# Optimization experiments

Hardware: AMD Instinct MI355X
Metric: run time of the kernel (lower is better)

Reference implementation:

```python
import jax, jax.numpy as jnp
import numpy as np

N_NODES = 100000
N_EDGES = 1600000
F_IN = 500
HIDDEN = 64
N_CLASS = 40


def gcn_conv(x, W, b, src, dst, n_nodes):
    """PyG GCNConv: add self-loops, symmetric deg^-1/2 normalization,
    linear transform then scatter-add aggregation at dst."""
    h = x @ W  # [N, out]
    loop = jnp.arange(n_nodes, dtype=src.dtype)
    s = jnp.concatenate([src, loop])  # sources incl. self-loops
    d = jnp.concatenate([dst, loop])
    deg = jax.ops.segment_sum(jnp.ones_like(d, dtype=h.dtype), d, num_segments=n_nodes)
    dinv = jnp.where(deg > 0, jax.lax.rsqrt(deg), 0.0)
    norm = dinv[s] * dinv[d]  # [E+N]
    msg = h[s] * norm[:, None]  # gather + scale, [E+N, out]
    out = jax.ops.segment_sum(msg, d, num_segments=n_nodes)
    return out + b


def setup_inputs() -> dict:
    key = jax.random.key(0)
    k1, k2, k3, k4 = jax.random.split(key, 4)
    x = jax.random.normal(k1, (N_NODES, F_IN), dtype=jnp.float32)
    edge_index = jax.random.randint(k2, (2, N_EDGES), 0, N_NODES, dtype=jnp.int64)
    # Glorot-style init for GCNConv weights
    W1 = jax.random.normal(k3, (F_IN, HIDDEN), dtype=jnp.float32) / np.sqrt(F_IN)
    b1 = jnp.zeros((HIDDEN,), dtype=jnp.float32)
    W2 = jax.random.normal(k4, (HIDDEN, N_CLASS), dtype=jnp.float32) / np.sqrt(HIDDEN)
    b2 = jnp.zeros((N_CLASS,), dtype=jnp.float32)
    return {"x": x, "W1": W1, "b1": b1, "W2": W2, "b2": b2, "edge_index": edge_index}


def reference(x, W1, b1, W2, b2, edge_index):
    src, dst = edge_index[0], edge_index[1]
    n = x.shape[0]
    h = jax.nn.relu(gcn_conv(x, W1, b1, src, dst, n))
    # dropout is identity in eval mode (F.dropout with training=False)
    out = gcn_conv(h, W2, b2, src, dst, n)
    return jax.nn.log_softmax(out, axis=1)
```

## Files before the change

### kernel.cpp

```cpp
#include <hip/hip_runtime.h>
#include <math.h>

#define N_NODES 100000
#define N_EDGES 1600000
#define F_IN    500
#define HIDDEN  64
#define N_CLASS 40
#define KPAD    512

#define NB   2048
#define NPB  49
#define EPB  16384
#define CAP  1536

typedef __attribute__((ext_vector_type(4))) float f32x4;
typedef __attribute__((ext_vector_type(8))) __bf16 bf16x8;

__device__ __forceinline__ unsigned short f2bf(float f) {
    unsigned int u = __float_as_uint(f);
    u = (u + 0x7FFF + ((u >> 16) & 1)) >> 16;
    return (unsigned short)u;
}
__device__ __forceinline__ unsigned int packbf(float a, float b) {
    return (unsigned int)f2bf(a) | ((unsigned int)f2bf(b) << 16);
}
__device__ __forceinline__ float bfu_lo(unsigned int v) {
    return __uint_as_float(v << 16);
}
__device__ __forceinline__ float bfu_hi(unsigned int v) {
    return __uint_as_float(v & 0xFFFF0000u);
}

__global__ void k_prep_w1t(const float* __restrict__ w1, unsigned short* __restrict__ w1t,
                           int* __restrict__ bcnt) {
    int idx = blockIdx.x * blockDim.x + threadIdx.x;
    if (idx < NB) bcnt[idx] = 0;
    if (idx >= HIDDEN * KPAD) return;
    int n = idx >> 9, k = idx & (KPAD - 1);
    float v = (k < F_IN) ? w1[k * HIDDEN + n] : 0.f;
    w1t[idx] = f2bf(v);
}

__launch_bounds__(1024)
__global__ void k_bhist(const int* __restrict__ dst, int* __restrict__ bcnt, int e) {
    __shared__ int h[NB];
    for (int i = threadIdx.x; i < NB; i += 1024) h[i] = 0;
    __syncthreads();
    int base = blockIdx.x * EPB;
#pragma unroll
    for (int j = 0; j < 16; ++j) {
        int i = base + j * 1024 + threadIdx.x;
        if (i < e) atomicAdd(&h[dst[i] / NPB], 1);
    }
    __syncthreads();
    for (int i = threadIdx.x; i < NB; i += 1024)
        if (h[i]) atomicAdd(&bcnt[i], h[i]);
}

__launch_bounds__(1024)
__global__ void k_bscan(const int* __restrict__ bcnt, int* __restrict__ bptr,
                        int* __restrict__ bcur) {
    __shared__ int s[1024];
    int t = threadIdx.x;
    int a = bcnt[2 * t], b = bcnt[2 * t + 1];
    int v = a + b;
    s[t] = v;
    __syncthreads();
    for (int off = 1; off < 1024; off <<= 1) {
        int u = (t >= off) ? s[t - off] : 0;
        __syncthreads();
        s[t] += u;
        __syncthreads();
    }
    int excl = s[t] - v;
    bptr[2 * t] = excl;     bptr[2 * t + 1] = excl + a;
    bcur[2 * t] = excl;     bcur[2 * t + 1] = excl + a;
    if (t == 1023) bptr[NB] = s[1023];
}

__launch_bounds__(1024)
__global__ void k_bfill(const int* __restrict__ src, const int* __restrict__ dst,
                        int* __restrict__ bcur, int2* __restrict__ ebuf, int e) {
    __shared__ int hist[NB];
    __shared__ int base_[NB];
    for (int i = threadIdx.x; i < NB; i += 1024) hist[i] = 0;
    __syncthreads();
    int b0 = blockIdx.x * EPB;
    int s_[16], d_[16];
#pragma unroll
    for (int j = 0; j < 16; ++j) {
        int i = b0 + j * 1024 + threadIdx.x;
        if (i < e) {
            s_[j] = src[i];
            d_[j] = dst[i];
            atomicAdd(&hist[d_[j] / NPB], 1);
        } else d_[j] = -1;
    }
    __syncthreads();
    for (int i = threadIdx.x; i < NB; i += 1024) {
        int hc = hist[i];
        base_[i] = hc ? atomicAdd(&bcur[i], hc) : 0;
        hist[i] = 0;
    }
    __syncthreads();
#pragma unroll
    for (int j = 0; j < 16; ++j) {
        if (d_[j] >= 0) {
            int bu = d_[j] / NPB;
            int r = atomicAdd(&hist[bu], 1);
            ebuf[base_[bu] + r] = make_int2(s_[j], d_[j]);
        }
    }
}

__launch_bounds__(256)
__global__ void k_bucket_csr(const int2* __restrict__ ebuf, const int* __restrict__ bptr,
                             int* __restrict__ rp, int* __restrict__ col,
                             float* __restrict__ dinv, int n) {
    int b  = blockIdx.x;
    int lo = b * NPB;
    if (lo >= n) return;
    int hi  = min(lo + NPB, n);
    int eb0 = bptr[b], ec = bptr[b + 1] - eb0;

    __shared__ int2 pairs[CAP];
    __shared__ int  hist[NPB];
    __shared__ int  excl[NPB + 1];
    for (int j = threadIdx.x; j < NPB; j += 256) hist[j] = 0;
    __syncthreads();
    for (int i = threadIdx.x; i < ec; i += 256) {
        int2 p = ebuf[eb0 + i];
        if (i < CAP) pairs[i] = p;
        atomicAdd(&hist[p.y - lo], 1);
    }
    __syncthreads();
    if (threadIdx.x == 0) {
        int acc = 0;
        for (int j = 0; j < NPB; ++j) { excl[j] = acc; acc += hist[j]; }
        excl[NPB] = acc;
    }
    __syncthreads();
    for (int j = threadIdx.x; j < hi - lo; j += 256) {
        rp[lo + j]   = eb0 + excl[j];
        dinv[lo + j] = rsqrtf((float)(hist[j] + 1));
    }
    if (hi == n && threadIdx.x == 0) rp[n] = eb0 + ec;
    __syncthreads();
    for (int j = threadIdx.x; j < NPB; j += 256) hist[j] = 0;
    __syncthreads();
    for (int i = threadIdx.x; i < ec; i += 256) {
        int2 p  = (i < CAP) ? pairs[i] : ebuf[eb0 + i];
        int  li = p.y - lo;
        int  r  = atomicAdd(&hist[li], 1);
        col[eb0 + excl[li] + r] = p.x;
    }
}

__launch_bounds__(256)
__global__ void k_gemm1(const float* __restrict__ x, const unsigned short* __restrict__ w1t,
                        const float* __restrict__ dinv, unsigned short* __restrict__ hs, int n) {
    const int tid  = threadIdx.x;
    const int wave = tid >> 6;
    const int lane = tid & 63;
    const int quad = lane >> 4;
    const int l16  = lane & 15;
    const int rowb = blockIdx.x * 64 + wave * 16;

    const int  row = rowb + l16;
    const bool vr  = row < n;
    const float* p = &x[(size_t)(vr ? row : 0) * F_IN];
    const float4 z4 = make_float4(0.f, 0.f, 0.f, 0.f);

    f32x4 acc[4];
#pragma unroll
    for (int ct = 0; ct < 4; ++ct) acc[ct] = (f32x4)0.f;

    auto COMPUTE = [&](int ks, const float4& ca, const float4& cb) {
        bf16x8 bfrag[4];
#pragma unroll
        for (int ct = 0; ct < 4; ++ct)
            bfrag[ct] = *(const bf16x8*)&w1t[(ct * 16 + l16) * KPAD + ks * 32 + quad * 8];
        union { bf16x8 v; unsigned int u[4]; } af;
        af.u[0] = packbf(ca.x, ca.y); af.u[1] = packbf(ca.z, ca.w);
        af.u[2] = packbf(cb.x, cb.y); af.u[3] = packbf(cb.z, cb.w);
#pragma unroll
        for (int ct = 0; ct < 4; ++ct)
            acc[ct] = __builtin_amdgcn_mfma_f32_16x16x32_bf16(af.v, bfrag[ct], acc[ct], 0, 0, 0);
    };

    float4 ca, cb, na, nb;
    {
        const int c0 = quad * 8;
        ca = vr ? *(const float4*)&p[c0]     : z4;
        cb = vr ? *(const float4*)&p[c0 + 4] : z4;
    }
    for (int ks = 0; ks < 14; ++ks) {
        const int c1 = (ks + 1) * 32 + quad * 8;
        na = vr ? *(const float4*)&p[c1]     : z4;
        nb = vr ? *(const float4*)&p[c1 + 4] : z4;
        COMPUTE(ks, ca, cb);
        ca = na; cb = nb;
    }
    {
        const int c1 = 480 + quad * 8;
        const bool cv0 = (c1 + 4 <= F_IN);
        const bool cv1 = (c1 + 8 <= F_IN);
        na = (vr && cv0) ? *(const float4*)&p[c1]     : z4;
        nb = (vr && cv1) ? *(const float4*)&p[c1 + 4] : z4;
        COMPUTE(14, ca, cb);
        ca = na; cb = nb;
    }
    COMPUTE(15, ca, cb);

#pragma unroll
    for (int reg = 0; reg < 4; ++reg) {
        int grow = rowb + quad * 4 + reg;
        if (grow < n) {
            float dv = dinv[grow];
#pragma unroll
            for (int ct = 0; ct < 4; ++ct)
                hs[(size_t)grow * HIDDEN + ct * 16 + l16] = f2bf(dv * acc[ct][reg]);
        }
    }
}

template <int F, bool RELU, bool LSM>
__launch_bounds__(256)
__global__ void k_agg(const uint2* __restrict__ hs2, const int* __restrict__ rp,
                      const int* __restrict__ col, const float* __restrict__ dinv,
                      const float* __restrict__ bias, float* __restrict__ out, int n) {
    constexpr int PW2 = F / 4;
    const int lane = threadIdx.x & 63;
    const int q    = lane >> 4;
    const int p    = lane & 15;
    const bool act = p < PW2;
    int wid = __builtin_amdgcn_readfirstlane((blockIdx.x * blockDim.x + threadIdx.x) >> 6);
    const int nw = (gridDim.x * blockDim.x) >> 6;

    for (; wid < n; wid += nw) {
        const int beg = rp[wid], end = rp[wid + 1];
        float a0 = 0.f, a1 = 0.f, a2 = 0.f, a3 = 0.f;
        int e = beg + q;
        for (; e + 12 < end; e += 16) {
            int c0 = col[e], c1 = col[e + 4], c2 = col[e + 8], c3 = col[e + 12];
            uint2 v0 = act ? hs2[(unsigned)c0 * PW2 + p] : make_uint2(0u, 0u);
            uint2 v1 = act ? hs2[(unsigned)c1 * PW2 + p] : make_uint2(0u, 0u);
            uint2 v2 = act ? hs2[(unsigned)c2 * PW2 + p] : make_uint2(0u, 0u);
            uint2 v3 = act ? hs2[(unsigned)c3 * PW2 + p] : make_uint2(0u, 0u);
            a0 += bfu_lo(v0.x) + bfu_lo(v1.x) + bfu_lo(v2.x) + bfu_lo(v3.x);
            a1 += bfu_hi(v0.x) + bfu_hi(v1.x) + bfu_hi(v2.x) + bfu_hi(v3.x);
            a2 += bfu_lo(v0.y) + bfu_lo(v1.y) + bfu_lo(v2.y) + bfu_lo(v3.y);
            a3 += bfu_hi(v0.y) + bfu_hi(v1.y) + bfu_hi(v2.y) + bfu_hi(v3.y);
        }
        if (e + 4 < end) {
            int c0 = col[e], c1 = col[e + 4];
            uint2 v0 = act ? hs2[(unsigned)c0 * PW2 + p] : make_uint2(0u, 0u);
            uint2 v1 = act ? hs2[(unsigned)c1 * PW2 + p] : make_uint2(0u, 0u);
            a0 += bfu_lo(v0.x) + bfu_lo(v1.x);
            a1 += bfu_hi(v0.x) + bfu_hi(v1.x);
            a2 += bfu_lo(v0.y) + bfu_lo(v1.y);
            a3 += bfu_hi(v0.y) + bfu_hi(v1.y);
            e += 8;
        }
        if (e < end) {
            int c0 = col[e];
            uint2 v0 = act ? hs2[(unsigned)c0 * PW2 + p] : make_uint2(0u, 0u);
            a0 += bfu_lo(v0.x); a1 += bfu_hi(v0.x);
            a2 += bfu_lo(v0.y); a3 += bfu_hi(v0.y);
        }
        a0 += __shfl_xor(a0, 16); a1 += __shfl_xor(a1, 16);
        a2 += __shfl_xor(a2, 16); a3 += __shfl_xor(a3, 16);
        a0 += __shfl_xor(a0, 32); a1 += __shfl_xor(a1, 32);
        a2 += __shfl_xor(a2, 32); a3 += __shfl_xor(a3, 32);

        const float di = dinv[wid];
        uint2 sv  = act ? hs2[(unsigned)wid * PW2 + p] : make_uint2(0u, 0u);
        float4 bv = act ? *(const float4*)&bias[4 * p] : make_float4(0.f, 0.f, 0.f, 0.f);
        float r0 = di * (a0 + bfu_lo(sv.x)) + bv.x;
        float r1 = di * (a1 + bfu_hi(sv.x)) + bv.y;
        float r2 = di * (a2 + bfu_lo(sv.y)) + bv.z;
        float r3 = di * (a3 + bfu_hi(sv.y)) + bv.w;
        if (RELU) {
            r0 = fmaxf(r0, 0.f); r1 = fmaxf(r1, 0.f);
            r2 = fmaxf(r2, 0.f); r3 = fmaxf(r3, 0.f);
        }
        if (LSM) {
            float m = act ? fmaxf(fmaxf(r0, r1), fmaxf(r2, r3)) : -INFINITY;
#pragma unroll
            for (int off = 8; off; off >>= 1) m = fmaxf(m, __shfl_xor(m, off));
            float ex = act ? (__expf(r0 - m) + __expf(r1 - m) + __expf(r2 - m) + __expf(r3 - m))
                           : 0.f;
#pragma unroll
            for (int off = 8; off; off >>= 1) ex += __shfl_xor(ex, off);
            float lse = m + __logf(ex);
            r0 -= lse; r1 -= lse; r2 -= lse; r3 -= lse;
        }
        if (q == 0 && act)
            *(float4*)&out[(size_t)wid * F + 4 * p] = make_float4(r0, r1, r2, r3);
    }
}

__launch_bounds__(256)
__global__ void k_gemm2(const float* __restrict__ a, const float* __restrict__ w,
                        const float* __restrict__ dinv, unsigned short* __restrict__ out, int n) {
    __shared__ float ws[HIDDEN * N_CLASS];
    for (int idx = threadIdx.x; idx < HIDDEN * N_CLASS; idx += 256) ws[idx] = w[idx];
    __syncthreads();
    int idx = blockIdx.x * 256 + threadIdx.x;
    if (idx >= n * N_CLASS) return;
    int i = idx / N_CLASS, j = idx - i * N_CLASS;
    float s = 0.f;
#pragma unroll
    for (int k = 0; k < HIDDEN; k += 4) {
        float4 xv = *(const float4*)&a[(size_t)i * HIDDEN + k];
        s = fmaf(xv.x, ws[k * N_CLASS + j], s);
        s = fmaf(xv.y, ws[(k + 1) * N_CLASS + j], s);
        s = fmaf(xv.z, ws[(k + 2) * N_CLASS + j], s);
        s = fmaf(xv.w, ws[(k + 3) * N_CLASS + j], s);
    }
    out[idx] = f2bf(dinv[i] * s);
}

extern "C" void kernel_launch(void* const* d_in, const int* in_sizes, int n_in,
                              void* d_out, int out_size, void* d_ws, size_t ws_size,
                              hipStream_t stream) {
    const float* x   = (const float*)d_in[0];
    const float* W1  = (const float*)d_in[1];
    const float* b1  = (const float*)d_in[2];
    const float* W2  = (const float*)d_in[3];
    const float* b2  = (const float*)d_in[4];
    const int*   ei  = (const int*)d_in[5];
    const int*   src = ei;
    const int*   dst = ei + N_EDGES;
    float*       out = (float*)d_out;

    char*  ws  = (char*)d_ws;
    size_t off = 0;
    auto alloc = [&](size_t bytes) -> void* {
        void* p = ws + off;
        off += (bytes + 255) & ~(size_t)255;
        return p;
    };
    int*            bcnt = (int*)alloc((size_t)NB * 4);
    int*            bptr = (int*)alloc((size_t)(NB + 1) * 4);
    int*            bcur = (int*)alloc((size_t)NB * 4);
    int*            rp   = (int*)alloc((size_t)(N_NODES + 1) * 4);
    int*            col  = (int*)alloc((size_t)N_EDGES * 4);
    float*          dinv = (float*)alloc((size_t)N_NODES * 4);
    unsigned short* w1t  = (unsigned short*)alloc((size_t)HIDDEN * KPAD * 2);
    unsigned short* h1s  = (unsigned short*)alloc((size_t)N_NODES * HIDDEN * 2);
    float*          h1a  = (float*)alloc((size_t)N_NODES * HIDDEN * 4);
    int2*           ebuf = (int2*)h1a;
    unsigned short* h2s  = h1s;

    const int NBH = (N_EDGES + EPB - 1) / EPB;

    k_prep_w1t<<<(HIDDEN * KPAD + 255) / 256, 256, 0, stream>>>(W1, w1t, bcnt);
    k_bhist<<<NBH, 1024, 0, stream>>>(dst, bcnt, N_EDGES);
    k_bscan<<<1, 1024, 0, stream>>>(bcnt, bptr, bcur);
    k_bfill<<<NBH, 1024, 0, stream>>>(src, dst, bcur, ebuf, N_EDGES);
    k_bucket_csr<<<NB, 256, 0, stream>>>(ebuf, bptr, rp, col, dinv, N_NODES);

    k_gemm1<<<(N_NODES + 63) / 64, 256, 0, stream>>>(x, w1t, dinv, h1s, N_NODES);
    k_agg<HIDDEN, true, false><<<2048, 256, 0, stream>>>(
        (const uint2*)h1s, rp, col, dinv, b1, h1a, N_NODES);

    k_gemm2<<<(N_NODES * N_CLASS + 255) / 256, 256, 0, stream>>>(h1a, W2, dinv, h2s, N_NODES);
    k_agg<N_CLASS, false, true><<<2048, 256, 0, stream>>>(
        (const uint2*)h2s, rp, col, dinv, b2, out, N_NODES);
}
```

Baseline: 526.4 us.

## Stage W1 in LDS and deepen x prefetch in first GEMM

```diff
diff --git a/kernel.cpp b/kernel.cpp
--- a/kernel.cpp
+++ b/kernel.cpp
@@ -156,16 +156,31 @@
     }
 }
 
-__launch_bounds__(256)
+__launch_bounds__(512)
 __global__ void k_gemm1(const float* __restrict__ x, const unsigned short* __restrict__ w1t,
                         const float* __restrict__ dinv, unsigned short* __restrict__ hs, int n) {
+    constexpr int LDW = 520;
+    __shared__ __align__(16) unsigned short w1l[HIDDEN * LDW];
+
     const int tid  = threadIdx.x;
     const int wave = tid >> 6;
     const int lane = tid & 63;
     const int quad = lane >> 4;
     const int l16  = lane & 15;
-    const int rowb = blockIdx.x * 64 + wave * 16;
-
+
+    {
+        const uint4* g = (const uint4*)w1t;
+#pragma unroll
+        for (int i = 0; i < 8; ++i) {
+            int c   = i * 512 + tid;
+            int row = c >> 6, cc = c & 63;
+            uint4 v = g[c];
+            *(uint4*)&w1l[row * LDW + cc * 8] = v;
+        }
+    }
+    __syncthreads();
+
+    const int rowb = blockIdx.x * 128 + wave * 16;
     const int  row = rowb + l16;
     const bool vr  = row < n;
     const float* p = &x[(size_t)(vr ? row : 0) * F_IN];
@@ -175,42 +190,37 @@
 #pragma unroll
     for (int ct = 0; ct < 4; ++ct) acc[ct] = (f32x4)0.f;
 
-    auto COMPUTE = [&](int ks, const float4& ca, const float4& cb) {
+    float4 xa[3], xb[3];
+    auto XLOAD = [&](int ks) {
+        const int c0 = ks * 32 + quad * 8;
+        if (ks < 15) {
+            xa[ks % 3] = vr ? *(const float4*)&p[c0]     : z4;
+            xb[ks % 3] = vr ? *(const float4*)&p[c0 + 4] : z4;
+        } else {
+            const bool cv0 = (c0 + 4 <= F_IN);
+            const bool cv1 = (c0 + 8 <= F_IN);
+            xa[ks % 3] = (vr && cv0) ? *(const float4*)&p[c0]     : z4;
+            xb[ks % 3] = (vr && cv1) ? *(const float4*)&p[c0 + 4] : z4;
+        }
+    };
+    XLOAD(0); XLOAD(1); XLOAD(2);
+
+#pragma unroll
+    for (int ks = 0; ks < 16; ++ks) {
         bf16x8 bfrag[4];
 #pragma unroll
         for (int ct = 0; ct < 4; ++ct)
-            bfrag[ct] = *(const bf16x8*)&w1t[(ct * 16 + l16) * KPAD + ks * 32 + quad * 8];
+            bfrag[ct] = *(const bf16x8*)&w1l[(ct * 16 + l16) * LDW + ks * 32 + quad * 8];
+        const float4 ca = xa[ks % 3];
+        const float4 cb = xb[ks % 3];
+        if (ks + 3 < 16) XLOAD(ks + 3);
         union { bf16x8 v; unsigned int u[4]; } af;
         af.u[0] = packbf(ca.x, ca.y); af.u[1] = packbf(ca.z, ca.w);
         af.u[2] = packbf(cb.x, cb.y); af.u[3] = packbf(cb.z, cb.w);
 #pragma unroll
         for (int ct = 0; ct < 4; ++ct)
             acc[ct] = __builtin_amdgcn_mfma_f32_16x16x32_bf16(af.v, bfrag[ct], acc[ct], 0, 0, 0);
-    };
-
-    float4 ca, cb, na, nb;
-    {
-        const int c0 = quad * 8;
-        ca = vr ? *(const float4*)&p[c0]     : z4;
-        cb = vr ? *(const float4*)&p[c0 + 4] : z4;
-    }
-    for (int ks = 0; ks < 14; ++ks) {
-        const int c1 = (ks + 1) * 32 + quad * 8;
-        na = vr ? *(const float4*)&p[c1]     : z4;
-        nb = vr ? *(const float4*)&p[c1 + 4] : z4;
-        COMPUTE(ks, ca, cb);
-        ca = na; cb = nb;
-    }
-    {
-        const int c1 = 480 + quad * 8;
-        const bool cv0 = (c1 + 4 <= F_IN);
-        const bool cv1 = (c1 + 8 <= F_IN);
-        na = (vr && cv0) ? *(const float4*)&p[c1]     : z4;
-        nb = (vr && cv1) ? *(const float4*)&p[c1 + 4] : z4;
-        COMPUTE(14, ca, cb);
-        ca = na; cb = nb;
-    }
-    COMPUTE(15, ca, cb);
+    }
 
 #pragma unroll
     for (int reg = 0; reg < 4; ++reg) {
@@ -361,7 +371,7 @@
     k_bfill<<<NBH, 1024, 0, stream>>>(src, dst, bcur, ebuf, N_EDGES);
     k_bucket_csr<<<NB, 256, 0, stream>>>(ebuf, bptr, rp, col, dinv, N_NODES);
 
-    k_gemm1<<<(N_NODES + 63) / 64, 256, 0, stream>>>(x, w1t, dinv, h1s, N_NODES);
+    k_gemm1<<<(N_NODES + 127) / 128, 512, 0, stream>>>(x, w1t, dinv, h1s, N_NODES);
     k_agg<HIDDEN, true, false><<<2048, 256, 0, stream>>>(
         (const uint2*)h1s, rp, col, dinv, b1, h1a, N_NODES);
 
```

Result: no change. 523.0 us (-0.6%).
